# Performance work log

Measured on AMD Instinct MI355X. Metric: run time of the kernel, lower is better.

The kernel has to match this reference:

```python
import jax, jax.numpy as jnp
import numpy as np

B, T, F, N = 262144, 3, 17, 8
EMBD = 32
DT = 0.2  # 25/5*0.04
EPS = 1e-8  # torch.cosine_similarity eps


def _mono(x, wi, bi, wo, bo):
    # monotonic_fun with increasing=False: relu(-Linear(x)) -> Linear
    h = jax.nn.relu(-(x @ wi.T + bi))  # (..., EMBD)
    return h @ wo.T + bo               # (..., 1)


def _cos(a, b):
    dot = jnp.sum(a * b, axis=-1)
    na = jnp.maximum(jnp.linalg.norm(a, axis=-1), EPS)
    nb = jnp.maximum(jnp.linalg.norm(b, axis=-1), EPS)
    return dot / (na * nb)


def _angle_clamp(vec, e, ang):
    # vec: (B,K,2), e: (B,2) -> keep forces within effective angle cone, sum over K
    keep = jnp.abs(_cos(e[:, None, :], vec)) > ang
    return jnp.sum(vec * keep[..., None], axis=1)


def setup_inputs() -> dict:
    key = jax.random.key(0)
    ks = jax.random.split(key, 8)
    ego = jax.random.normal(ks[0], (B, T, F), jnp.float32)
    ego = ego.at[:, :, 2:4].multiply(10.0)  # position scale
    nei = jax.random.normal(ks[1], (B, N, F), jnp.float32)
    nei = nei.at[:, :, 2:4].multiply(10.0).at[:, :, 4:6].multiply(0.1)
    border = jax.random.normal(ks[2], (4,), jnp.float32)
    attr_dest_para = jax.random.uniform(ks[3], (2,), jnp.float32) + 0.1  # relu(rand), keep away from 0 divisor
    eff_angle = jax.nn.sigmoid(jax.random.uniform(ks[4], (1,), jnp.float32))

    def mlp(k):
        k1, k2, k3, k4 = jax.random.split(k, 4)
        wi = jax.random.uniform(k1, (EMBD, 1), jnp.float32)      # clamped >= 0
        bi = jax.random.normal(k2, (EMBD,), jnp.float32) * 0.1
        wo = jax.random.uniform(k3, (1, EMBD), jnp.float32) * 0.1  # clamped >= 0
        bo = jax.random.normal(k4, (1,), jnp.float32) * 0.1
        return wi, bi, wo, bo

    an = mlp(ks[5])
    rn = mlp(ks[6])
    rb = mlp(ks[7])
    dl = mlp(jax.random.fold_in(key, 99))
    return dict(
        ego=ego, nei=nei, border=border,
        attr_dest_para=attr_dest_para, eff_angle=eff_angle,
        an_wi=an[0], an_bi=an[1], an_wo=an[2], an_bo=an[3],
        rn_wi=rn[0], rn_bi=rn[1], rn_wo=rn[2], rn_bo=rn[3],
        rb_wi=rb[0], rb_bi=rb[1], rb_wo=rb[2], rb_bo=rb[3],
        dl_wi=dl[0], dl_bi=dl[1], dl_wo=dl[2], dl_bo=dl[3],
    )


def reference(ego, nei, border, attr_dest_para, eff_angle,
              an_wi, an_bi, an_wo, an_bo,
              rn_wi, rn_bi, rn_wo, rn_bo,
              rb_wi, rb_bi, rb_wo, rb_bo,
              dl_wi, dl_bi, dl_wo, dl_bo):
    ego_last = ego[:, -1]  # (B,F)

    # --- attr_destination (desired_velocity=None branch) ---
    v34 = ego_last[:, 3:5]
    dv = jnp.stack([jnp.linalg.norm(v34, axis=-1),
                    jnp.zeros(ego.shape[0], ego.dtype)], axis=1)  # (B,2)
    f_dest = ((attr_dest_para[1] * dv - v34) / attr_dest_para[0])[:, None, :]  # (B,1,2)

    # --- attr_repu_neighbors ---
    r = nei[:, :, 2:4] - ego_last[:, None, 2:4]  # (B,N,2)
    mask = nei[:, :, 2:4] == 0                    # (B,N,2)
    r_norm = jnp.linalg.norm(r, axis=-1, keepdims=True)  # (B,N,1)

    # neighbor durality: quirky use of batch element 1, shared across batch
    ids_last = ego[1, -1, 8:-1]  # (8,) neighbor-id columns
    dur = jnp.zeros(N, ego.dtype)
    for t in range(ego.shape[1]):
        dur = dur + jnp.isin(ids_last, ego[1, t, 8:-1]).astype(ego.dtype)

    f_attr = _mono(r_norm, an_wi, an_bi, an_wo, an_bo) * r / r_norm \
             * _mono(dur[:, None], dl_wi, dl_bi, dl_wo, dl_bo)  # (B,N,2)*(N,1)
    f_attr = jnp.where(mask, 0.0, f_attr)

    v_nei = nei[:, :, 4:6]
    b = r_norm \
        + jnp.sum((r + v_nei * DT) ** 2, axis=-1, keepdims=True) \
        - jnp.sum((v_nei * DT) ** 2, axis=-1, keepdims=True)
    b = jnp.sqrt(b) / 2
    f_repu = _mono(b, rn_wi, rn_bi, rn_wo, rn_bo) * r / r_norm
    f_repu = jnp.where(mask, 0.0, f_repu)

    # --- repu_borders (select_lane = [0, -1]) ---
    rb_all = ego_last[:, 3, None] - border        # (B,4)
    rbv = jnp.stack([rb_all[:, 0], rb_all[:, -1]], axis=1)  # (B,2)
    rbn = jnp.abs(rbv)
    f_bor = _mono(rbn[..., None], rb_wi, rb_bi, rb_wo, rb_bo) * (rbv / rbn)[..., None]  # (B,2,1)
    f_bor = jnp.concatenate([jnp.zeros_like(f_bor), f_bor], axis=-1)  # (B,2,2): [0, fy]

    # --- angle clamp + integrate ---
    e = ego_last[:, 4:6]
    e = e / jnp.linalg.norm(e, axis=1, keepdims=True)
    a = (_angle_clamp(f_dest, e, eff_angle)
         + _angle_clamp(f_attr, e, eff_angle) + _angle_clamp(f_repu, e, eff_angle)
         + _angle_clamp(f_bor, e, eff_angle))
    v = ego_last[:, 2:4] + a * DT
    s = ego_last[:, :2] + v * DT
    return jnp.concatenate([s, v, a], axis=1)  # (B,6)
```

## Files before the change

kernel.cpp:

```cpp
#include <hip/hip_runtime.h>

#define DTC 0.2f
#define EPSC 1e-8f


__global__ __launch_bounds__(128) void sfm_pre(
    const float* __restrict__ ego,
    const float* __restrict__ an_wi, const float* __restrict__ an_bi, const float* __restrict__ an_wo,
    const float* __restrict__ rn_wi, const float* __restrict__ rn_bi, const float* __restrict__ rn_wo,
    const float* __restrict__ rb_wi, const float* __restrict__ rb_bi, const float* __restrict__ rb_wo,
    const float* __restrict__ dl_wi, const float* __restrict__ dl_bi,
    const float* __restrict__ dl_wo, const float* __restrict__ dl_bo,
    float* __restrict__ ws)
{
    __shared__ float tk[96], wiwo[96], wobi[96], skn[96], ssw[96], ssb[96];
    int t = threadIdx.x;
    if (t < 96) {
        int f = t >> 5, k = t & 31;
        const float* wip = (f == 0) ? an_wi : ((f == 1) ? rn_wi : rb_wi);
        const float* bip = (f == 0) ? an_bi : ((f == 1) ? rn_bi : rb_bi);
        const float* wop = (f == 0) ? an_wo : ((f == 1) ? rn_wo : rb_wo);
        float wi = wip[k], bi = bip[k], wo = wop[k];
        tk[t]   = -bi / wi;
        wiwo[t] = wi * wo;
        wobi[t] = wo * bi;
    }
    __syncthreads();
    if (t < 96) {
        int f = t >> 5, k = t & 31;
        float my = tk[t];
        int rank = 0;
        for (int m = 0; m < 32; ++m) {
            float o = tk[f * 32 + m];
            rank += (o < my || (o == my && m < k)) ? 1 : 0;
        }
        skn[f * 32 + rank] = my;
        ssw[f * 32 + rank] = wiwo[t];
        ssb[f * 32 + rank] = wobi[t];
    }
    __syncthreads();
    if (t < 96) {
        int f = t >> 5, p = t & 31;
        float sw_ = 0.f, sb_ = 0.f;
        for (int m = p; m < 32; ++m) { sw_ += ssw[f * 32 + m]; sb_ += ssb[f * 32 + m]; }
        int base = 16 + f * 112;
        ws[base + p]      = skn[f * 32 + p];
        ws[base + 32 + p] = sw_;
        ws[base + 65 + p] = sb_;
        if (p == 0) { ws[base + 64] = 0.f; ws[base + 97] = 0.f; }
    }
    if (t >= 96 && t < 104) {
        int j = t - 96;
        const float* base = ego + 51;
        float idv = base[2 * 17 + 8 + j];
        float dur = 0.f;
        for (int tt = 0; tt < 3; ++tt) {
            bool fo = false;
            for (int m = 0; m < 8; ++m) fo = fo || (idv == base[tt * 17 + 8 + m]);
            dur += fo ? 1.f : 0.f;
        }
        float acc = 0.f;
        for (int k = 0; k < 32; ++k)
            acc = fmaf(dl_wo[k], fmaxf(0.f, -fmaf(dl_wi[k], dur, dl_bi[k])), acc);
        ws[j] = acc + dl_bo[0];
    }
}

__device__ __forceinline__ float mono_eval(const float* __restrict__ kn, float x) {
    int i = (kn[15] <= x) ? 16 : 0;
    i += (kn[i + 7] <= x) ? 8 : 0;
    i += (kn[i + 3] <= x) ? 4 : 0;
    i += (kn[i + 1] <= x) ? 2 : 0;
    i += (kn[i] <= x) ? 1 : 0;
    return -fmaf(kn[32 + i], x, kn[65 + i]);
}

__global__ __launch_bounds__(256) void sfm_main(
    const float* __restrict__ ego, const float* __restrict__ nei,
    const float* __restrict__ border, const float* __restrict__ adp,
    const float* __restrict__ eang,
    const float* __restrict__ an_bo, const float* __restrict__ rn_bo,
    const float* __restrict__ rb_bo,
    const float* __restrict__ wsrc,
    float* __restrict__ out, int Bn)
{
    __shared__ float sw[360];
    int t = threadIdx.x;
    for (int i = t; i < 352; i += 256) sw[i] = wsrc[i];
    if (t == 0) sw[352] = an_bo[0];
    if (t == 1) sw[353] = rn_bo[0];
    if (t == 2) sw[354] = rb_bo[0];
    if (t == 3) sw[355] = adp[0];
    if (t == 4) sw[356] = adp[1];
    if (t == 5) sw[357] = eang[0];
    if (t == 6) sw[358] = border[0];
    if (t == 7) sw[359] = border[3];
    __syncthreads();

    int l = t & 7;
    long long row = (long long)blockIdx.x * 32 + (t >> 3);
    if (row >= Bn) return;

    float egv = 0.f;
    if (l < 6) egv = ego[row * 51 + 34 + l];
    int lb = (t & 63) & ~7;
    float g0 = __shfl(egv, lb + 0, 64);
    float g1 = __shfl(egv, lb + 1, 64);
    float g2 = __shfl(egv, lb + 2, 64);
    float g3 = __shfl(egv, lb + 3, 64);
    float g4 = __shfl(egv, lb + 4, 64);
    float g5 = __shfl(egv, lb + 5, 64);

    const float* nr = nei + row * 136 + l * 17 + 2;
    float nx = nr[0], ny = nr[1], vx = nr[2], vy = nr[3];

    float Rx = nx - g2, Ry = ny - g3;
    float rr = sqrtf(Rx * Rx + Ry * Ry);
    float ax = fmaf(vx, DTC, Rx), ay = fmaf(vy, DTC, Ry);
    float wx = vx * DTC, wy = vy * DTC;
    float bb = sqrtf(rr + ax * ax + ay * ay - wx * wx - wy * wy) * 0.5f;

    float an_bo_v = sw[352], rn_bo_v = sw[353], rb_bo_v = sw[354];
    float p0 = sw[355], p1 = sw[356], ang = sw[357];
    float rb0 = g3 - sw[358], rb1 = g3 - sw[359];
    float rbn0 = fabsf(rb0), rbn1 = fabsf(rb1);

    float fA = mono_eval(sw + 16, rr) + an_bo_v;
    float fR = mono_eval(sw + 128, bb) + rn_bo_v;
    float xb = (l == 1) ? rbn1 : rbn0;
    float vB = 0.f;
    if (l < 2) vB = mono_eval(sw + 240, xb) + rb_bo_v;
    float vB0 = __shfl(vB, lb + 0, 64);
    float vB1 = __shfl(vB, lb + 1, 64);

    float elen = sqrtf(g4 * g4 + g5 * g5);
    float ex = g4 / elen, ey = g5 / elen;
    float na = fmaxf(sqrtf(ex * ex + ey * ey), EPSC);

    float axs = 0.f, ays = 0.f;
#define CLAMP_ADD(VX, VY)                                                   \
    {                                                                       \
        float _vx = (VX), _vy = (VY);                                       \
        float _nv = fmaxf(sqrtf(_vx * _vx + _vy * _vy), EPSC);              \
        float _c = (ex * _vx + ey * _vy) / (na * _nv);                      \
        if (fabsf(_c) > ang) { axs += _vx; ays += _vy; }                    \
    }

    float mfx = (nx == 0.f) ? 0.f : 1.f;
    float mfy = (ny == 0.f) ? 0.f : 1.f;

    {
        float coef = fA / rr * sw[l];
        CLAMP_ADD(coef * Rx * mfx, coef * Ry * mfy);
    }
    {
        float coef = fR / rr;
        CLAMP_ADD(coef * Rx * mfx, coef * Ry * mfy);
    }

#pragma unroll
    for (int m = 1; m < 8; m <<= 1) {
        axs += __shfl_xor(axs, m, 64);
        ays += __shfl_xor(ays, m, 64);
    }

    if (l == 0) {
        float dvn = sqrtf(g3 * g3 + g4 * g4);
        CLAMP_ADD((p1 * dvn - g3) / p0, -g4 / p0);
        CLAMP_ADD(0.f, vB0 * (rb0 / rbn0));
        CLAMP_ADD(0.f, vB1 * (rb1 / rbn1));

        float vxo = fmaf(axs, DTC, g2);
        float vyo = fmaf(ays, DTC, g3);
        float* op = out + row * 6;
        op[0] = fmaf(vxo, DTC, g0);
        op[1] = fmaf(vyo, DTC, g1);
        op[2] = vxo; op[3] = vyo;
        op[4] = axs; op[5] = ays;
    }
#undef CLAMP_ADD
}

extern "C" void kernel_launch(void* const* d_in, const int* in_sizes, int n_in,
                              void* d_out, int out_size, void* d_ws, size_t ws_size,
                              hipStream_t stream) {
    const float* ego    = (const float*)d_in[0];
    const float* nei    = (const float*)d_in[1];
    const float* border = (const float*)d_in[2];
    const float* adp    = (const float*)d_in[3];
    const float* eang   = (const float*)d_in[4];
    const float* an_wi  = (const float*)d_in[5];
    const float* an_bi  = (const float*)d_in[6];
    const float* an_wo  = (const float*)d_in[7];
    const float* an_bo  = (const float*)d_in[8];
    const float* rn_wi  = (const float*)d_in[9];
    const float* rn_bi  = (const float*)d_in[10];
    const float* rn_wo  = (const float*)d_in[11];
    const float* rn_bo  = (const float*)d_in[12];
    const float* rb_wi  = (const float*)d_in[13];
    const float* rb_bi  = (const float*)d_in[14];
    const float* rb_wo  = (const float*)d_in[15];
    const float* rb_bo  = (const float*)d_in[16];
    const float* dl_wi  = (const float*)d_in[17];
    const float* dl_bi  = (const float*)d_in[18];
    const float* dl_wo  = (const float*)d_in[19];
    const float* dl_bo  = (const float*)d_in[20];
    float* out = (float*)d_out;
    float* ws  = (float*)d_ws;

    int Bn = in_sizes[0] / (3 * 17);

    sfm_pre<<<1, 128, 0, stream>>>(ego,
                                   an_wi, an_bi, an_wo,
                                   rn_wi, rn_bi, rn_wo,
                                   rb_wi, rb_bi, rb_wo,
                                   dl_wi, dl_bi, dl_wo, dl_bo, ws);

    int grid = (Bn + 31) / 32;
    sfm_main<<<grid, 256, 0, stream>>>(ego, nei, border, adp, eang,
                                       an_bo, rn_bo, rb_bo,
                                       ws, out, Bn);
}
```

Baseline: 280.4 us.

## Fuse the weight-preprocessing kernel into the main kernel, recomputing per block

Drops the separate single-block preprocessing launch. Every block of the main kernel now sorts the piecewise-linear knots, builds the suffix sums and evaluates the duration MLP itself in shared memory. The per-row neighbor and ego loads are issued before this setup so their latency overlaps the preprocessing work. This removes one launch and the serial dependency through global workspace, at the cost of redundant per-block setup work and two extra barriers in each of the 8192 blocks.

New measurement: 285.8 us. About the same (+1.9%).

```diff
diff --git a/kernel.cpp b/kernel.cpp
--- a/kernel.cpp
+++ b/kernel.cpp
@@ -3,51 +3,51 @@
 #define DTC 0.2f
 #define EPSC 1e-8f
 
-
-__global__ __launch_bounds__(128) void sfm_pre(
-    const float* __restrict__ ego,
-    const float* __restrict__ an_wi, const float* __restrict__ an_bi, const float* __restrict__ an_wo,
-    const float* __restrict__ rn_wi, const float* __restrict__ rn_bi, const float* __restrict__ rn_wo,
-    const float* __restrict__ rb_wi, const float* __restrict__ rb_bi, const float* __restrict__ rb_wo,
+__device__ __forceinline__ float mono_eval(const float* __restrict__ kn, float x) {
+    int i = (kn[15] <= x) ? 16 : 0;
+    i += (kn[i + 7] <= x) ? 8 : 0;
+    i += (kn[i + 3] <= x) ? 4 : 0;
+    i += (kn[i + 1] <= x) ? 2 : 0;
+    i += (kn[i] <= x) ? 1 : 0;
+    return -fmaf(kn[32 + i], x, kn[65 + i]);
+}
+
+__global__ __launch_bounds__(256) void sfm_fused(
+    const float* __restrict__ ego, const float* __restrict__ nei,
+    const float* __restrict__ border, const float* __restrict__ adp,
+    const float* __restrict__ eang,
+    const float* __restrict__ an_wi, const float* __restrict__ an_bi,
+    const float* __restrict__ an_wo, const float* __restrict__ an_bo,
+    const float* __restrict__ rn_wi, const float* __restrict__ rn_bi,
+    const float* __restrict__ rn_wo, const float* __restrict__ rn_bo,
+    const float* __restrict__ rb_wi, const float* __restrict__ rb_bi,
+    const float* __restrict__ rb_wo, const float* __restrict__ rb_bo,
     const float* __restrict__ dl_wi, const float* __restrict__ dl_bi,
     const float* __restrict__ dl_wo, const float* __restrict__ dl_bo,
-    float* __restrict__ ws)
+    float* __restrict__ out, int Bn)
 {
-    __shared__ float tk[96], wiwo[96], wobi[96], skn[96], ssw[96], ssb[96];
+    __shared__ float sw[360];
+    __shared__ float tk[96], w1[96], w2[96], sk[96], s1[96], s2[96];
+
     int t = threadIdx.x;
+    int l = t & 7;
+    long long row = (long long)blockIdx.x * 32 + (t >> 3);
+    long long prow = (row < Bn) ? row : (long long)(Bn - 1);
+
+    const float* nr = nei + prow * 136 + l * 17 + 2;
+    float nx = nr[0], ny = nr[1], vx = nr[2], vy = nr[3];
+    float egv = 0.f;
+    if (l < 6) egv = ego[prow * 51 + 34 + l];
+
     if (t < 96) {
         int f = t >> 5, k = t & 31;
         const float* wip = (f == 0) ? an_wi : ((f == 1) ? rn_wi : rb_wi);
         const float* bip = (f == 0) ? an_bi : ((f == 1) ? rn_bi : rb_bi);
         const float* wop = (f == 0) ? an_wo : ((f == 1) ? rn_wo : rb_wo);
         float wi = wip[k], bi = bip[k], wo = wop[k];
-        tk[t]   = -bi / wi;
-        wiwo[t] = wi * wo;
-        wobi[t] = wo * bi;
-    }
-    __syncthreads();
-    if (t < 96) {
-        int f = t >> 5, k = t & 31;
-        float my = tk[t];
-        int rank = 0;
-        for (int m = 0; m < 32; ++m) {
-            float o = tk[f * 32 + m];
-            rank += (o < my || (o == my && m < k)) ? 1 : 0;
-        }
-        skn[f * 32 + rank] = my;
-        ssw[f * 32 + rank] = wiwo[t];
-        ssb[f * 32 + rank] = wobi[t];
-    }
-    __syncthreads();
-    if (t < 96) {
-        int f = t >> 5, p = t & 31;
-        float sw_ = 0.f, sb_ = 0.f;
-        for (int m = p; m < 32; ++m) { sw_ += ssw[f * 32 + m]; sb_ += ssb[f * 32 + m]; }
-        int base = 16 + f * 112;
-        ws[base + p]      = skn[f * 32 + p];
-        ws[base + 32 + p] = sw_;
-        ws[base + 65 + p] = sb_;
-        if (p == 0) { ws[base + 64] = 0.f; ws[base + 97] = 0.f; }
+        tk[t] = -bi / wi;
+        w1[t] = wi * wo;
+        w2[t] = wo * bi;
     }
     if (t >= 96 && t < 104) {
         int j = t - 96;
@@ -60,125 +60,127 @@
             dur += fo ? 1.f : 0.f;
         }
         float acc = 0.f;
+#pragma unroll
         for (int k = 0; k < 32; ++k)
             acc = fmaf(dl_wo[k], fmaxf(0.f, -fmaf(dl_wi[k], dur, dl_bi[k])), acc);
-        ws[j] = acc + dl_bo[0];
-    }
-}
-
-__device__ __forceinline__ float mono_eval(const float* __restrict__ kn, float x) {
-    int i = (kn[15] <= x) ? 16 : 0;
-    i += (kn[i + 7] <= x) ? 8 : 0;
-    i += (kn[i + 3] <= x) ? 4 : 0;
-    i += (kn[i + 1] <= x) ? 2 : 0;
-    i += (kn[i] <= x) ? 1 : 0;
-    return -fmaf(kn[32 + i], x, kn[65 + i]);
-}
-
-__global__ __launch_bounds__(256) void sfm_main(
-    const float* __restrict__ ego, const float* __restrict__ nei,
-    const float* __restrict__ border, const float* __restrict__ adp,
-    const float* __restrict__ eang,
-    const float* __restrict__ an_bo, const float* __restrict__ rn_bo,
-    const float* __restrict__ rb_bo,
-    const float* __restrict__ wsrc,
-    float* __restrict__ out, int Bn)
-{
-    __shared__ float sw[360];
-    int t = threadIdx.x;
-    for (int i = t; i < 352; i += 256) sw[i] = wsrc[i];
-    if (t == 0) sw[352] = an_bo[0];
-    if (t == 1) sw[353] = rn_bo[0];
-    if (t == 2) sw[354] = rb_bo[0];
-    if (t == 3) sw[355] = adp[0];
-    if (t == 4) sw[356] = adp[1];
-    if (t == 5) sw[357] = eang[0];
-    if (t == 6) sw[358] = border[0];
-    if (t == 7) sw[359] = border[3];
+        sw[j] = acc + dl_bo[0];
+    }
+    if (t == 104) sw[352] = an_bo[0];
+    if (t == 105) sw[353] = rn_bo[0];
+    if (t == 106) sw[354] = rb_bo[0];
+    if (t == 107) sw[355] = adp[0];
+    if (t == 108) sw[356] = adp[1];
+    if (t == 109) sw[357] = eang[0];
+    if (t == 110) sw[358] = border[0];
+    if (t == 111) sw[359] = border[3];
     __syncthreads();
 
-    int l = t & 7;
-    long long row = (long long)blockIdx.x * 32 + (t >> 3);
-    if (row >= Bn) return;
-
-    float egv = 0.f;
-    if (l < 6) egv = ego[row * 51 + 34 + l];
-    int lb = (t & 63) & ~7;
-    float g0 = __shfl(egv, lb + 0, 64);
-    float g1 = __shfl(egv, lb + 1, 64);
-    float g2 = __shfl(egv, lb + 2, 64);
-    float g3 = __shfl(egv, lb + 3, 64);
-    float g4 = __shfl(egv, lb + 4, 64);
-    float g5 = __shfl(egv, lb + 5, 64);
-
-    const float* nr = nei + row * 136 + l * 17 + 2;
-    float nx = nr[0], ny = nr[1], vx = nr[2], vy = nr[3];
-
-    float Rx = nx - g2, Ry = ny - g3;
-    float rr = sqrtf(Rx * Rx + Ry * Ry);
-    float ax = fmaf(vx, DTC, Rx), ay = fmaf(vy, DTC, Ry);
-    float wx = vx * DTC, wy = vy * DTC;
-    float bb = sqrtf(rr + ax * ax + ay * ay - wx * wx - wy * wy) * 0.5f;
-
-    float an_bo_v = sw[352], rn_bo_v = sw[353], rb_bo_v = sw[354];
-    float p0 = sw[355], p1 = sw[356], ang = sw[357];
-    float rb0 = g3 - sw[358], rb1 = g3 - sw[359];
-    float rbn0 = fabsf(rb0), rbn1 = fabsf(rb1);
-
-    float fA = mono_eval(sw + 16, rr) + an_bo_v;
-    float fR = mono_eval(sw + 128, bb) + rn_bo_v;
-    float xb = (l == 1) ? rbn1 : rbn0;
-    float vB = 0.f;
-    if (l < 2) vB = mono_eval(sw + 240, xb) + rb_bo_v;
-    float vB0 = __shfl(vB, lb + 0, 64);
-    float vB1 = __shfl(vB, lb + 1, 64);
-
-    float elen = sqrtf(g4 * g4 + g5 * g5);
-    float ex = g4 / elen, ey = g5 / elen;
-    float na = fmaxf(sqrtf(ex * ex + ey * ey), EPSC);
-
-    float axs = 0.f, ays = 0.f;
+    if (t < 96) {
+        int k = t & 31, b = t & ~31;
+        float my = tk[t];
+        int rank = 0;
+#pragma unroll
+        for (int m = 0; m < 32; ++m) {
+            float o = tk[b + m];
+            rank += (o < my || (o == my && m < k)) ? 1 : 0;
+        }
+        sk[b + rank] = my;
+        s1[b + rank] = w1[t];
+        s2[b + rank] = w2[t];
+    }
+    __syncthreads();
+
+    if (t < 96) {
+        int f = t >> 5, p = t & 31, b = t & ~31;
+        float sw_ = 0.f, sb_ = 0.f;
+#pragma unroll
+        for (int m = 0; m < 32; ++m) {
+            float a = s1[b + m], c = s2[b + m];
+            if (m >= p) { sw_ += a; sb_ += c; }
+        }
+        int base = 16 + f * 112;
+        sw[base + p]      = sk[b + p];
+        sw[base + 32 + p] = sw_;
+        sw[base + 65 + p] = sb_;
+        if (p == 0) { sw[base + 64] = 0.f; sw[base + 97] = 0.f; }
+    }
+    __syncthreads();
+
+    if (row < Bn) {
+        int lb = (t & 63) & ~7;
+        float g0 = __shfl(egv, lb + 0, 64);
+        float g1 = __shfl(egv, lb + 1, 64);
+        float g2 = __shfl(egv, lb + 2, 64);
+        float g3 = __shfl(egv, lb + 3, 64);
+        float g4 = __shfl(egv, lb + 4, 64);
+        float g5 = __shfl(egv, lb + 5, 64);
+
+        float Rx = nx - g2, Ry = ny - g3;
+        float rr = sqrtf(Rx * Rx + Ry * Ry);
+        float ax = fmaf(vx, DTC, Rx), ay = fmaf(vy, DTC, Ry);
+        float wx = vx * DTC, wy = vy * DTC;
+        float bb = sqrtf(rr + ax * ax + ay * ay - wx * wx - wy * wy) * 0.5f;
+
+        float an_bo_v = sw[352], rn_bo_v = sw[353], rb_bo_v = sw[354];
+        float p0 = sw[355], p1 = sw[356], ang = sw[357];
+        float rb0 = g3 - sw[358], rb1 = g3 - sw[359];
+        float rbn0 = fabsf(rb0), rbn1 = fabsf(rb1);
+
+        float fA = mono_eval(sw + 16, rr) + an_bo_v;
+        float fR = mono_eval(sw + 128, bb) + rn_bo_v;
+        float xb = (l == 1) ? rbn1 : rbn0;
+        float vB = 0.f;
+        if (l < 2) vB = mono_eval(sw + 240, xb) + rb_bo_v;
+        float vB0 = __shfl(vB, lb + 0, 64);
+        float vB1 = __shfl(vB, lb + 1, 64);
+
+        float elen = sqrtf(g4 * g4 + g5 * g5);
+        float ex = g4 / elen, ey = g5 / elen;
+        float na = fmaxf(sqrtf(ex * ex + ey * ey), EPSC);
+
+        float axs = 0.f, ays = 0.f;
 #define CLAMP_ADD(VX, VY)                                                   \
-    {                                                                       \
-        float _vx = (VX), _vy = (VY);                                       \
-        float _nv = fmaxf(sqrtf(_vx * _vx + _vy * _vy), EPSC);              \
-        float _c = (ex * _vx + ey * _vy) / (na * _nv);                      \
-        if (fabsf(_c) > ang) { axs += _vx; ays += _vy; }                    \
-    }
-
-    float mfx = (nx == 0.f) ? 0.f : 1.f;
-    float mfy = (ny == 0.f) ? 0.f : 1.f;
-
-    {
-        float coef = fA / rr * sw[l];
-        CLAMP_ADD(coef * Rx * mfx, coef * Ry * mfy);
-    }
-    {
-        float coef = fR / rr;
-        CLAMP_ADD(coef * Rx * mfx, coef * Ry * mfy);
-    }
-
-#pragma unroll
-    for (int m = 1; m < 8; m <<= 1) {
-        axs += __shfl_xor(axs, m, 64);
-        ays += __shfl_xor(ays, m, 64);
-    }
-
-    if (l == 0) {
-        float dvn = sqrtf(g3 * g3 + g4 * g4);
-        CLAMP_ADD((p1 * dvn - g3) / p0, -g4 / p0);
-        CLAMP_ADD(0.f, vB0 * (rb0 / rbn0));
-        CLAMP_ADD(0.f, vB1 * (rb1 / rbn1));
-
-        float vxo = fmaf(axs, DTC, g2);
-        float vyo = fmaf(ays, DTC, g3);
-        float* op = out + row * 6;
-        op[0] = fmaf(vxo, DTC, g0);
-        op[1] = fmaf(vyo, DTC, g1);
-        op[2] = vxo; op[3] = vyo;
-        op[4] = axs; op[5] = ays;
-    }
+        {                                                                   \
+            float _vx = (VX), _vy = (VY);                                   \
+            float _nv = fmaxf(sqrtf(_vx * _vx + _vy * _vy), EPSC);          \
+            float _c = (ex * _vx + ey * _vy) / (na * _nv);                  \
+            if (fabsf(_c) > ang) { axs += _vx; ays += _vy; }                \
+        }
+
+        float mfx = (nx == 0.f) ? 0.f : 1.f;
+        float mfy = (ny == 0.f) ? 0.f : 1.f;
+
+        {
+            float coef = fA / rr * sw[l];
+            CLAMP_ADD(coef * Rx * mfx, coef * Ry * mfy);
+        }
+        {
+            float coef = fR / rr;
+            CLAMP_ADD(coef * Rx * mfx, coef * Ry * mfy);
+        }
+
+#pragma unroll
+        for (int m = 1; m < 8; m <<= 1) {
+            axs += __shfl_xor(axs, m, 64);
+            ays += __shfl_xor(ays, m, 64);
+        }
+
+        if (l == 0) {
+            float dvn = sqrtf(g3 * g3 + g4 * g4);
+            CLAMP_ADD((p1 * dvn - g3) / p0, -g4 / p0);
+            CLAMP_ADD(0.f, vB0 * (rb0 / rbn0));
+            CLAMP_ADD(0.f, vB1 * (rb1 / rbn1));
+
+            float vxo = fmaf(axs, DTC, g2);
+            float vyo = fmaf(ays, DTC, g3);
+            float* op = out + row * 6;
+            op[0] = fmaf(vxo, DTC, g0);
+            op[1] = fmaf(vyo, DTC, g1);
+            op[2] = vxo; op[3] = vyo;
+            op[4] = axs; op[5] = ays;
+        }
 #undef CLAMP_ADD
+    }
 }
 
 extern "C" void kernel_launch(void* const* d_in, const int* in_sizes, int n_in,
@@ -206,18 +208,14 @@
     const float* dl_wo  = (const float*)d_in[19];
     const float* dl_bo  = (const float*)d_in[20];
     float* out = (float*)d_out;
-    float* ws  = (float*)d_ws;
+    (void)d_ws; (void)ws_size;
 
     int Bn = in_sizes[0] / (3 * 17);
-
-    sfm_pre<<<1, 128, 0, stream>>>(ego,
-                                   an_wi, an_bi, an_wo,
-                                   rn_wi, rn_bi, rn_wo,
-                                   rb_wi, rb_bi, rb_wo,
-                                   dl_wi, dl_bi, dl_wo, dl_bo, ws);
-
     int grid = (Bn + 31) / 32;
-    sfm_main<<<grid, 256, 0, stream>>>(ego, nei, border, adp, eang,
-                                       an_bo, rn_bo, rb_bo,
-                                       ws, out, Bn);
+    sfm_fused<<<grid, 256, 0, stream>>>(ego, nei, border, adp, eang,
+                                        an_wi, an_bi, an_wo, an_bo,
+                                        rn_wi, rn_bi, rn_wo, rn_bo,
+                                        rb_wi, rb_bi, rb_wo, rb_bo,
+                                        dl_wi, dl_bi, dl_wo, dl_bo,
+                                        out, Bn);
 }
```
